# Kernel tuning notes

Measured on AMD Instinct MI355X. Metric: run time of the kernel, lower is better.

Reference implementation:

```python
import jax, jax.numpy as jnp
import numpy as np

SEP_THRESHOLD = 5.0
TEMPERATURE = 0.1          # sigmoid temperature
SCALING_FACTOR = 1.0
DIST_TEMPERATURE = 1.0     # exponential temperature for repulsion energy
ATT_LOSS_GATE = 0.0
REP_LOSS_GATE = 0.0
EPS = 1e-10


def setup_inputs() -> dict:
    key = jax.random.key(0)
    k1, k2 = jax.random.split(key)
    B, L, K, C, D = 16, 64, 32, 32, 512
    prior = jax.random.normal(k1, (B, L, K, C), dtype=jnp.float32)
    h = jax.random.normal(k2, (B, L, D), dtype=jnp.float32)
    return {"prior": prior, "h": h}


def _jsd_matrix(prior):
    # prior: (B, L, K, C) logits -> pairwise JSD summed over K factors: (B, L, L)
    logp = jax.nn.log_softmax(prior, axis=-1)          # (B,L,K,C)
    p = jnp.exp(logp)
    p1, p2 = p[:, :, None], p[:, None]                  # (B,L,1,K,C), (B,1,L,K,C)
    lp1, lp2 = logp[:, :, None], logp[:, None]
    logm = jnp.log(0.5 * (p1 + p2))                     # mixture log-probs
    kl_p_m = jnp.sum(p1 * (lp1 - logm), axis=-1)        # (B,L,L,K)
    kl_q_m = jnp.sum(p2 * (lp2 - logm), axis=-1)
    jsd = 0.5 * (kl_p_m + kl_q_m)
    return jsd.sum(axis=-1) * SCALING_FACTOR            # (B,L,L)


def _ste_mask(soft, hard, triu):
    # straight-through: hard values forward, soft gradient backward
    return (hard + soft - jax.lax.stop_gradient(soft)) * triu


def reference(prior, h):
    B, L, K, C = prior.shape
    jsd = _jsd_matrix(prior)                            # (B,L,L)

    triu = jnp.triu(jnp.ones((L, L), dtype=prior.dtype), k=1)
    soft_att = jax.nn.sigmoid((SEP_THRESHOLD - jsd) / TEMPERATURE)
    hard_att = (jsd < SEP_THRESHOLD).astype(prior.dtype)
    att_mask = _ste_mask(soft_att, hard_att, triu)
    soft_rep = jax.nn.sigmoid((jsd - SEP_THRESHOLD) / TEMPERATURE)
    hard_rep = (jsd >= SEP_THRESHOLD).astype(prior.dtype)
    rep_mask = _ste_mask(soft_rep, hard_rep, triu)

    # pairwise MSE over hidden dim: (B,L,L)
    diff = h[:, :, None, :] - h[:, None, :, :]
    pairwise_mse = jnp.mean(diff * diff, axis=-1)

    loss_att = (pairwise_mse * att_mask).sum() / (att_mask.sum() + EPS)
    loss_att = jnp.where(loss_att > ATT_LOSS_GATE, loss_att, 0.0)

    repulsion_energy = jnp.exp(-pairwise_mse / DIST_TEMPERATURE)
    loss_rep = (repulsion_energy * rep_mask).sum() / (rep_mask.sum() + EPS)
    loss_rep = jnp.where(loss_rep > REP_LOSS_GATE, loss_rep, 0.0)

    return loss_att, loss_rep
```

## Files before the change

kernel.cpp:

```cpp
#include <hip/hip_runtime.h>
#include <math.h>

#define NB 16
#define NL 64
#define NK 32
#define NC 32
#define ND 512
#define EPSF 1e-10f

#define TILES_PER_B 36
#define PAIR_BLOCKS (NB * TILES_PER_B * 2)

#define THRS 14.426950408889634f
#define L2E  1.4426950408889634f

typedef _Float16 half2v __attribute__((ext_vector_type(2)));
typedef _Float16 half4v __attribute__((ext_vector_type(4)));
typedef _Float16 half8v __attribute__((ext_vector_type(8)));


__global__ void __launch_bounds__(256) softmax_kernel(
        const float* __restrict__ prior,
        const float* __restrict__ hg,
        _Float16* __restrict__ P,
        float2* __restrict__ H2,
        _Float16* __restrict__ h16) {
    int bl = blockIdx.x;
    int t  = threadIdx.x;

    const float* src = prior + (size_t)bl * (NK * NC);
    float4 x = *(const float4*)(src + t * 4);
    float y0 = x.x * L2E, y1 = x.y * L2E, y2 = x.z * L2E, y3 = x.w * L2E;

    float m = fmaxf(fmaxf(y0, y1), fmaxf(y2, y3));
    #pragma unroll
    for (int w = 4; w >= 1; w >>= 1)
        m = fmaxf(m, __shfl_xor(m, w, 8));

    float e0 = exp2f(y0 - m), e1 = exp2f(y1 - m);
    float e2 = exp2f(y2 - m), e3 = exp2f(y3 - m);
    float s = e0 + e1 + e2 + e3;
    #pragma unroll
    for (int w = 4; w >= 1; w >>= 1)
        s += __shfl_xor(s, w, 8);

    float rs = 1.0f / s;
    float ls = __log2f(s);
    float p0 = e0 * rs, p1 = e1 * rs, p2 = e2 * rs, p3 = e3 * rs;
    float l0 = (y0 - m) - ls, l1 = (y1 - m) - ls;
    float l2 = (y2 - m) - ls, l3 = (y3 - m) - ls;

    half4v pv;
    pv[0] = (_Float16)fmaxf(p0, 1e-6f);
    pv[1] = (_Float16)fmaxf(p1, 1e-6f);
    pv[2] = (_Float16)fmaxf(p2, 1e-6f);
    pv[3] = (_Float16)fmaxf(p3, 1e-6f);
    *(half4v*)(P + (size_t)bl * (NK * NC) + t * 4) = pv;

    float2 hv = *(const float2*)(hg + (size_t)bl * ND + t * 2);
    half2v hh; hh[0] = (_Float16)hv.x; hh[1] = (_Float16)hv.y;
    *(half2v*)(h16 + (size_t)bl * ND + t * 2) = hh;

    float hacc = p0 * l0 + p1 * l1 + p2 * l2 + p3 * l3;
    #pragma unroll
    for (int w = 32; w >= 1; w >>= 1)
        hacc += __shfl_xor(hacc, w);
    __shared__ float red[4];
    int lane = t & 63, wib = t >> 6;
    if (lane == 0) red[wib] = hacc;
    __syncthreads();
    if (t == 0)
        H2[bl] = make_float2(red[0] + red[1], red[2] + red[3]);
}

template<int CTRL>
__device__ __forceinline__ float dpp_add(float x) {
    int yi = __builtin_amdgcn_update_dpp(0, __float_as_int(x), CTRL, 0xF, 0xF, true);
    return x + __int_as_float(yi);
}

__device__ __forceinline__ float bf4f(float v0, float v1, float v2, float v3,
                                      bool hi32, bool hi16) {
    float sel0 = hi32 ? v2 : v0, oth0 = hi32 ? v0 : v2;
    float sel1 = hi32 ? v3 : v1, oth1 = hi32 ? v1 : v3;
    float w0 = sel0 + __shfl_xor(oth0, 32);
    float w1 = sel1 + __shfl_xor(oth1, 32);
    float sel = hi16 ? w1 : w0, oth = hi16 ? w0 : w1;
    float x = sel + __shfl_xor(oth, 16);
    x = dpp_add<0x111>(x);
    x = dpp_add<0x112>(x);
    x = dpp_add<0x114>(x);
    x = dpp_add<0x118>(x);
    return x;
}

__global__ void __launch_bounds__(256) pair_kernel(
        const _Float16* __restrict__ P,
        const float2* __restrict__ H2g,
        const _Float16* __restrict__ h16,
        float* __restrict__ partials) {
    __shared__ float red[4][4];

    int tid  = threadIdx.x;
    int lane = tid & 63;
    int wv   = tid >> 6;

    int wg    = blockIdx.x;
    int b     = wg / (TILES_PER_B * 2);
    int rem72 = wg % (TILES_PER_B * 2);
    int t36   = rem72 >> 1;
    int half  = rem72 & 1;

    int ti = 0, rem = t36;
    while (rem >= 8 - ti) { rem -= 8 - ti; ++ti; }
    int tj = ti + rem;
    bool diag = (ti == tj);
    int bi0 = b * NL + ti * 8;
    int bj0 = b * NL + tj * 8;

    int r = half * 4 + wv;

    const _Float16* arow = P + (size_t)(bi0 + r) * (NK * NC);
    half8v ar1 = *(const half8v*)(arow + lane * 8);
    half8v ar2 = *(const half8v*)(arow + 512 + lane * 8);
    half8v hr  = *(const half8v*)(h16 + (size_t)(bi0 + r) * ND + lane * 8);
    float2 h2i = H2g[bi0 + r];

    const _Float16* Pj = P   + (size_t)bj0 * (NK * NC);
    const _Float16* Hj = h16 + (size_t)bj0 * ND;

    bool hi32 = (lane & 32) != 0;
    bool hi16 = (lane & 16) != 0;
    int  sgrp = lane >> 4;
    bool actl = (lane & 15) == 15;

    float S[8], M[8];
    #pragma unroll
    for (int s = 0; s < 8; ++s) {
        half8v b1 = *(const half8v*)(Pj + s * 1024 + lane * 8);
        half8v t1 = ar1 + b1;
        float a0 = 0.f, a1 = 0.f;
        #pragma unroll
        for (int e = 0; e < 8; e += 2) {
            float f0 = (float)t1[e];     a0 = fmaf(f0, __log2f(f0), a0);
            float f1 = (float)t1[e + 1]; a1 = fmaf(f1, __log2f(f1), a1);
        }
        S[s] = a0 + a1;

        half8v hs = *(const half8v*)(Hj + s * 512 + lane * 8);
        half8v d = hr - hs;
        float m0 = 0.f, m1 = 0.f;
        #pragma unroll
        for (int e = 0; e < 8; e += 2) {
            m0 = fmaf((float)d[e],     (float)d[e],     m0);
            m1 = fmaf((float)d[e + 1], (float)d[e + 1], m1);
        }
        M[s] = m0 + m1;
    }

    float xSA0 = bf4f(S[0], S[1], S[2], S[3], hi32, hi16);
    float xSA1 = bf4f(S[4], S[5], S[6], S[7], hi32, hi16);
    float xM0  = bf4f(M[0], M[1], M[2], M[3], hi32, hi16);
    float xM1  = bf4f(M[4], M[5], M[6], M[7], hi32, hi16);

    int s0 = sgrp, s1 = 4 + sgrp;
    float2 h2j0 = H2g[bj0 + s0];
    float2 h2j1 = H2g[bj0 + s1];
    float statA0 = h2i.x + h2j0.x + 32.0f - xSA0;
    float statA1 = h2i.x + h2j1.x + 32.0f - xSA1;
    bool valid0 = (!diag) || (s0 > r);
    bool valid1 = (!diag) || (s1 > r);
    float stat0 = statA0, stat1 = statA1;

    if (__any(actl && valid0 && (statA0 < THRS))) {
        float SB[4];
        #pragma unroll
        for (int q = 0; q < 4; ++q) {
            half8v b2 = *(const half8v*)(Pj + q * 1024 + 512 + lane * 8);
            half8v t2 = ar2 + b2;
            float a0 = 0.f, a1 = 0.f;
            #pragma unroll
            for (int e = 0; e < 8; e += 2) {
                float g0 = (float)t2[e];     a0 = fmaf(g0, __log2f(g0), a0);
                float g1 = (float)t2[e + 1]; a1 = fmaf(g1, __log2f(g1), a1);
            }
            SB[q] = a0 + a1;
        }
        float xSB = bf4f(SB[0], SB[1], SB[2], SB[3], hi32, hi16);
        stat0 = statA0 + (h2i.y + h2j0.y + 32.0f - xSB);
    }
    if (__any(actl && valid1 && (statA1 < THRS))) {
        float SB[4];
        #pragma unroll
        for (int q = 0; q < 4; ++q) {
            half8v b2 = *(const half8v*)(Pj + (q + 4) * 1024 + 512 + lane * 8);
            half8v t2 = ar2 + b2;
            float a0 = 0.f, a1 = 0.f;
            #pragma unroll
            for (int e = 0; e < 8; e += 2) {
                float g0 = (float)t2[e];     a0 = fmaf(g0, __log2f(g0), a0);
                float g1 = (float)t2[e + 1]; a1 = fmaf(g1, __log2f(g1), a1);
            }
            SB[q] = a0 + a1;
        }
        float xSB = bf4f(SB[0], SB[1], SB[2], SB[3], hi32, hi16);
        stat1 = statA1 + (h2i.y + h2j1.y + 32.0f - xSB);
    }

    float mse0 = xM0 * (1.0f / ND);
    float mse1 = xM1 * (1.0f / ND);
    float rt0  = exp2f(-mse0 * L2E);
    float rt1  = exp2f(-mse1 * L2E);
    bool att0 = stat0 < THRS;
    bool att1 = stat1 < THRS;

    float attN = 0.f, attC = 0.f, repN = 0.f, repC = 0.f;
    attN += (actl && valid0 && att0)  ? mse0 : 0.f;
    attC += (actl && valid0 && att0)  ? 1.f  : 0.f;
    repN += (actl && valid0 && !att0) ? rt0  : 0.f;
    repC += (actl && valid0 && !att0) ? 1.f  : 0.f;
    attN += (actl && valid1 && att1)  ? mse1 : 0.f;
    attC += (actl && valid1 && att1)  ? 1.f  : 0.f;
    repN += (actl && valid1 && !att1) ? rt1  : 0.f;
    repC += (actl && valid1 && !att1) ? 1.f  : 0.f;

    attN += __shfl_xor(attN, 16); attN += __shfl_xor(attN, 32);
    attC += __shfl_xor(attC, 16); attC += __shfl_xor(attC, 32);
    repN += __shfl_xor(repN, 16); repN += __shfl_xor(repN, 32);
    repC += __shfl_xor(repC, 16); repC += __shfl_xor(repC, 32);

    if (lane == 63) {
        red[wv][0] = attN; red[wv][1] = attC;
        red[wv][2] = repN; red[wv][3] = repC;
    }
    __syncthreads();
    if (tid < 4) {
        float v = red[0][tid] + red[1][tid] + red[2][tid] + red[3][tid];
        partials[blockIdx.x * 4 + tid] = v;
    }
}

__global__ void __launch_bounds__(256) finalize_kernel(
        const float* __restrict__ partials,
        float* __restrict__ out) {
    int tid = threadIdx.x;
    float a0 = 0.0f, a1 = 0.0f, a2 = 0.0f, a3 = 0.0f;
    for (int bkt = tid; bkt < PAIR_BLOCKS; bkt += 256) {
        a0 += partials[bkt * 4 + 0];
        a1 += partials[bkt * 4 + 1];
        a2 += partials[bkt * 4 + 2];
        a3 += partials[bkt * 4 + 3];
    }
    #pragma unroll
    for (int w = 32; w >= 1; w >>= 1) {
        a0 += __shfl_xor(a0, w);
        a1 += __shfl_xor(a1, w);
        a2 += __shfl_xor(a2, w);
        a3 += __shfl_xor(a3, w);
    }
    __shared__ float red[4][4];
    int lane = tid & 63, wib = tid >> 6;
    if (lane == 0) {
        red[wib][0] = a0; red[wib][1] = a1; red[wib][2] = a2; red[wib][3] = a3;
    }
    __syncthreads();
    if (tid == 0) {
        float s0 = red[0][0] + red[1][0] + red[2][0] + red[3][0];
        float s1 = red[0][1] + red[1][1] + red[2][1] + red[3][1];
        float s2 = red[0][2] + red[1][2] + red[2][2] + red[3][2];
        float s3 = red[0][3] + red[1][3] + red[2][3] + red[3][3];
        float la = s0 / (s1 + EPSF);
        float lr = s2 / (s3 + EPSF);
        out[0] = (la > 0.0f) ? la : 0.0f;
        out[1] = (lr > 0.0f) ? lr : 0.0f;
    }
}

extern "C" void kernel_launch(void* const* d_in, const int* in_sizes, int n_in,
                              void* d_out, int out_size, void* d_ws, size_t ws_size,
                              hipStream_t stream) {
    const float* prior = (const float*)d_in[0];
    const float* h     = (const float*)d_in[1];
    float* out = (float*)d_out;
    float* ws  = (float*)d_ws;

    float* partials = ws;
    _Float16* P = (_Float16*)(ws + 8192);
    float2* H2 = (float2*)(ws + 8192 + 524288);
    _Float16* h16 = (_Float16*)(ws + 8192 + 524288 + 2048);

    softmax_kernel<<<NB * NL, 256, 0, stream>>>(prior, h, P, H2, h16);

    pair_kernel<<<PAIR_BLOCKS, 256, 0, stream>>>(P, H2, h16, partials);

    finalize_kernel<<<1, 256, 0, stream>>>(partials, out);
}
```

Measured before the change: 23.56 us.

## Compute pairwise MSE via MFMA Gram matrix instead of direct differences

Pairwise MSE is now computed with the identity |a|^2 + |b|^2 - 2a·b. A new gram_kernel uses 16x16x32 f16 MFMA on the fp16 hidden states, and the softmax kernel additionally produces squared norms. The pair kernel then reads precomputed MSE values instead of loading h rows and reducing differences. This removes the per-pair h loads and reductions, at the cost of an extra kernel launch, a global intermediate buffer, and possible cancellation error in the expanded form.

Result: slower. 27.14 us (+15.2%).

```diff
diff --git a/kernel.cpp b/kernel.cpp
--- a/kernel.cpp
+++ b/kernel.cpp
@@ -17,6 +17,7 @@
 typedef _Float16 half2v __attribute__((ext_vector_type(2)));
 typedef _Float16 half4v __attribute__((ext_vector_type(4)));
 typedef _Float16 half8v __attribute__((ext_vector_type(8)));
+typedef float   floatx4 __attribute__((ext_vector_type(4)));
 
 
 __global__ void __launch_bounds__(256) softmax_kernel(
@@ -24,7 +25,8 @@
         const float* __restrict__ hg,
         _Float16* __restrict__ P,
         float2* __restrict__ H2,
-        _Float16* __restrict__ h16) {
+        _Float16* __restrict__ h16,
+        float* __restrict__ Hn) {
     int bl = blockIdx.x;
     int t  = threadIdx.x;
 
@@ -60,17 +62,63 @@
     float2 hv = *(const float2*)(hg + (size_t)bl * ND + t * 2);
     half2v hh; hh[0] = (_Float16)hv.x; hh[1] = (_Float16)hv.y;
     *(half2v*)(h16 + (size_t)bl * ND + t * 2) = hh;
+    float f0 = (float)hh[0], f1 = (float)hh[1];
+    float hsq = f0 * f0 + f1 * f1;
 
     float hacc = p0 * l0 + p1 * l1 + p2 * l2 + p3 * l3;
     #pragma unroll
-    for (int w = 32; w >= 1; w >>= 1)
+    for (int w = 32; w >= 1; w >>= 1) {
         hacc += __shfl_xor(hacc, w);
+        hsq  += __shfl_xor(hsq, w);
+    }
     __shared__ float red[4];
+    __shared__ float redq[4];
     int lane = t & 63, wib = t >> 6;
-    if (lane == 0) red[wib] = hacc;
+    if (lane == 0) { red[wib] = hacc; redq[wib] = hsq; }
     __syncthreads();
-    if (t == 0)
+    if (t == 0) {
         H2[bl] = make_float2(red[0] + red[1], red[2] + red[3]);
+        Hn[bl] = redq[0] + redq[1] + redq[2] + redq[3];
+    }
+}
+
+__global__ void __launch_bounds__(256) gram_kernel(
+        const _Float16* __restrict__ h16,
+        const float* __restrict__ Hn,
+        float* __restrict__ mseG) {
+    int tid  = threadIdx.x;
+    int lane = tid & 63;
+    int wv   = tid >> 6;
+
+    int b  = blockIdx.x >> 2;
+    int si = blockIdx.x & 3;
+
+    int mrow = lane & 15;
+    int kgrp = lane >> 4;
+
+    const _Float16* Arow = h16 + ((size_t)(b * NL + si * 16 + mrow)) * ND + kgrp * 8;
+    const _Float16* Brow = h16 + ((size_t)(b * NL + wv * 16 + mrow)) * ND + kgrp * 8;
+
+    floatx4 acc = {0.f, 0.f, 0.f, 0.f};
+    #pragma unroll
+    for (int kk = 0; kk < 16; ++kk) {
+        half8v a  = *(const half8v*)(Arow + kk * 32);
+        half8v bb = *(const half8v*)(Brow + kk * 32);
+        acc = __builtin_amdgcn_mfma_f32_16x16x32_f16(a, bb, acc, 0, 0, 0);
+    }
+
+    int col = lane & 15;
+    const float* HnB = Hn + b * NL;
+    float hnj = HnB[wv * 16 + col];
+    float* dst = mseG + ((size_t)b << 12);
+    #pragma unroll
+    for (int reg = 0; reg < 4; ++reg) {
+        int row = (lane >> 4) * 4 + reg;
+        int i = si * 16 + row;
+        int j = wv * 16 + col;
+        float mse = (HnB[i] + hnj - 2.0f * acc[reg]) * (1.0f / ND);
+        dst[i * 64 + j] = mse;
+    }
 }
 
 template<int CTRL>
@@ -97,7 +145,7 @@
 __global__ void __launch_bounds__(256) pair_kernel(
         const _Float16* __restrict__ P,
         const float2* __restrict__ H2g,
-        const _Float16* __restrict__ h16,
+        const float* __restrict__ mseG,
         float* __restrict__ partials) {
     __shared__ float red[4][4];
 
@@ -123,18 +171,16 @@
     const _Float16* arow = P + (size_t)(bi0 + r) * (NK * NC);
     half8v ar1 = *(const half8v*)(arow + lane * 8);
     half8v ar2 = *(const half8v*)(arow + 512 + lane * 8);
-    half8v hr  = *(const half8v*)(h16 + (size_t)(bi0 + r) * ND + lane * 8);
     float2 h2i = H2g[bi0 + r];
 
-    const _Float16* Pj = P   + (size_t)bj0 * (NK * NC);
-    const _Float16* Hj = h16 + (size_t)bj0 * ND;
+    const _Float16* Pj = P + (size_t)bj0 * (NK * NC);
 
     bool hi32 = (lane & 32) != 0;
     bool hi16 = (lane & 16) != 0;
     int  sgrp = lane >> 4;
     bool actl = (lane & 15) == 15;
 
-    float S[8], M[8];
+    float S[8];
     #pragma unroll
     for (int s = 0; s < 8; ++s) {
         half8v b1 = *(const half8v*)(Pj + s * 1024 + lane * 8);
@@ -146,22 +192,10 @@
             float f1 = (float)t1[e + 1]; a1 = fmaf(f1, __log2f(f1), a1);
         }
         S[s] = a0 + a1;
-
-        half8v hs = *(const half8v*)(Hj + s * 512 + lane * 8);
-        half8v d = hr - hs;
-        float m0 = 0.f, m1 = 0.f;
-        #pragma unroll
-        for (int e = 0; e < 8; e += 2) {
-            m0 = fmaf((float)d[e],     (float)d[e],     m0);
-            m1 = fmaf((float)d[e + 1], (float)d[e + 1], m1);
-        }
-        M[s] = m0 + m1;
     }
 
     float xSA0 = bf4f(S[0], S[1], S[2], S[3], hi32, hi16);
     float xSA1 = bf4f(S[4], S[5], S[6], S[7], hi32, hi16);
-    float xM0  = bf4f(M[0], M[1], M[2], M[3], hi32, hi16);
-    float xM1  = bf4f(M[4], M[5], M[6], M[7], hi32, hi16);
 
     int s0 = sgrp, s1 = 4 + sgrp;
     float2 h2j0 = H2g[bj0 + s0];
@@ -171,6 +205,10 @@
     bool valid0 = (!diag) || (s0 > r);
     bool valid1 = (!diag) || (s1 > r);
     float stat0 = statA0, stat1 = statA1;
+
+    const float* mseB = mseG + ((size_t)b << 12) + (ti * 8 + r) * 64 + tj * 8;
+    float mse0 = mseB[s0];
+    float mse1 = mseB[s1];
 
     if (__any(actl && valid0 && (statA0 < THRS))) {
         float SB[4];
@@ -207,10 +245,8 @@
         stat1 = statA1 + (h2i.y + h2j1.y + 32.0f - xSB);
     }
 
-    float mse0 = xM0 * (1.0f / ND);
-    float mse1 = xM1 * (1.0f / ND);
-    float rt0  = exp2f(-mse0 * L2E);
-    float rt1  = exp2f(-mse1 * L2E);
+    float rt0 = exp2f(-mse0 * L2E);
+    float rt1 = exp2f(-mse1 * L2E);
     bool att0 = stat0 < THRS;
     bool att1 = stat1 < THRS;
 
@@ -288,10 +324,14 @@
     _Float16* P = (_Float16*)(ws + 8192);
     float2* H2 = (float2*)(ws + 8192 + 524288);
     _Float16* h16 = (_Float16*)(ws + 8192 + 524288 + 2048);
-
-    softmax_kernel<<<NB * NL, 256, 0, stream>>>(prior, h, P, H2, h16);
-
-    pair_kernel<<<PAIR_BLOCKS, 256, 0, stream>>>(P, H2, h16, partials);
+    float* Hn   = ws + 8192 + 524288 + 2048 + 262144;
+    float* mseG = Hn + 1024;
+
+    softmax_kernel<<<NB * NL, 256, 0, stream>>>(prior, h, P, H2, h16, Hn);
+
+    gram_kernel<<<NB * 4, 256, 0, stream>>>(h16, Hn, mseG);
+
+    pair_kernel<<<PAIR_BLOCKS, 256, 0, stream>>>(P, H2, mseG, partials);
 
     finalize_kernel<<<1, 256, 0, stream>>>(partials, out);
 }
```
